# Kernel optimization log

Measured on AMD Instinct MI355X. Metric: run time of the kernel, lower is better.

The kernel has to match this reference:

```python
import jax, jax.numpy as jnp
import numpy as np

PATCH = 8
EPS = 1e-5

def patch_split(x, s):
    # B C H W -> B s*s rH rW C
    B, C, H, W = x.shape
    rH, rW = H // s, W // s
    out = x.reshape(B, C, s, rH, s, rW)
    out = out.transpose(0, 2, 4, 3, 5, 1)
    return out.reshape(B, s * s, rH, rW, C)

def patch_recover(x, s):
    # B s*s rH rW C -> B C H W
    B, N, rH, rW, C = x.shape
    out = x.reshape(B, s, s, rH, rW, C)
    out = out.transpose(0, 5, 1, 3, 2, 4)
    return out.reshape(B, C, s * rH, s * rW)

def conv2d(x, w, pad):
    return jax.lax.conv_general_dilated(x, w, (1, 1), [(pad, pad), (pad, pad)],
                                        dimension_numbers=('NCHW', 'OIHW', 'NCHW'))

def bn_relu(x, g, b):
    # eval-mode BatchNorm2d with fresh running stats (mean=0, var=1)
    scale = (g / jnp.sqrt(1.0 + EPS))[None, :, None, None]
    return jax.nn.relu(x * scale + b[None, :, None, None])


def setup_inputs() -> dict:
    key = jax.random.key(0)
    ks = jax.random.split(key, 24)
    r = lambda i, shape, s=0.02: jax.random.normal(ks[i], shape, jnp.float32) * s
    B, H, W, C, K, P = 4, 64, 64, 512, 19, 64
    return {
        'M_1': jax.random.normal(ks[0], (B, 2048, H, W), jnp.float32),
        'F': jax.random.normal(ks[1], (B, C, H, W), jnp.float32),
        'I': jax.random.normal(ks[2], (B, K, H, W), jnp.float32),
        'R': jax.random.uniform(ks[3], (B, K, PATCH, PATCH), jnp.float32),
        'lg_w1': r(4, (P, P)), 'lg_w2': r(5, (C, C)),
        'fuse_w': r(6, (P,)), 'fuse_b': r(7, (1,)),
        'q_w': r(8, (256, C)), 'q_b': r(9, (256,)),
        'k_w': r(10, (256, C)), 'k_b': r(11, (256,)),
        'v_w': r(12, (256, C)), 'v_b': r(13, (256,)),
        'c1_w': r(14, (512, 256, 1, 1)),
        'bn1_g': jnp.ones((512,)), 'bn1_b': jnp.zeros((512,)),
        'c2_w': r(15, (512, 512, 3, 3)),
        'bn2_g': jnp.ones((512,)), 'bn2_b': jnp.zeros((512,)),
        'c3_w': r(16, (512, 2560, 3, 3)),
        'bn3_g': jnp.ones((512,)), 'bn3_b': jnp.zeros((512,)),
        'drop_w': r(17, (K, 512, 1, 1)),
    }


def reference(M_1, F, I, R, lg_w1, lg_w2, fuse_w, fuse_b, q_w, q_b, k_w, k_b,
              v_w, v_b, c1_w, bn1_g, bn1_b, c2_w, bn2_g, bn2_b, c3_w, bn3_g,
              bn3_b, drop_w):
    B = F.shape[0]
    F_p5 = patch_split(F, PATCH)          # B P rH rW C
    _, P, rH, rW, C = F_p5.shape
    I_p5 = patch_split(I, PATCH)          # B P rH rW K
    K = I_p5.shape[-1]
    F_p = F_p5.reshape(B, P, rH * rW, C)
    I_p = I_p5.reshape(B, P, rH * rW, K)
    bin_conf = R.reshape(B, K, P).transpose(0, 2, 1)[..., None]  # B P K 1
    pix = jax.nn.softmax(I_p, axis=2)
    F_l = jnp.einsum('bpnk,bpnc->bpkc', pix, F_p) * bin_conf     # B P K C
    # LG block: 1x1 conv over P channels, residual relu, linear over C
    h = jnp.einsum('qp,bpkc->bqkc', lg_w1, F_l)
    h = jax.nn.relu(h + F_l)
    F_l = jnp.einsum('bpkc,dc->bpkd', h, lg_w2)
    # FUSE: 1x1 conv P->1 (with bias); broadcast replaces torch .repeat
    F_g = jnp.einsum('p,bpkc->bkc', fuse_w, F_l) + fuse_b        # B K C
    query = jnp.einsum('bpnc,dc->bpnd', F_p, q_w) + q_b          # B P N 256
    key_ = jnp.einsum('bpkc,dc->bpkd', F_l, k_w) + k_b           # B P K 256
    value = jnp.einsum('bkc,dc->bkd', F_g, v_w) + v_b            # B K 256
    aff = jax.nn.softmax(jnp.einsum('bpnd,bpkd->bpnk', query, key_), axis=-1)
    F_s = jnp.einsum('bpnk,bkd->bpnd', aff, value)               # B P N 256
    F_s = patch_recover(F_s.reshape(B, P, rH, rW, -1), PATCH)    # B 256 H W
    Fo1 = F + bn_relu(conv2d(F_s, c1_w, 0), bn1_g, bn1_b)
    x2 = bn_relu(conv2d(Fo1, c2_w, 1), bn2_g, bn2_b)
    x3 = bn_relu(conv2d(jnp.concatenate([x2, M_1], axis=1), c3_w, 1), bn3_g, bn3_b)
    # Dropout2d is identity in eval; final 1x1 classifier conv
    return conv2d(x3, drop_w, 0)
```

## Files before the change

### kernel.cpp

```cpp
#include <hip/hip_runtime.h>
#include <hip/hip_bf16.h>

typedef __hip_bfloat16 bf16;
using short8 = __attribute__((ext_vector_type(8))) short;
using f32x4  = __attribute__((ext_vector_type(4))) float;

__device__ __forceinline__ float b2f(bf16 v){ return __bfloat162float(v); }
__device__ __forceinline__ bf16  f2b(float v){ return __float2bfloat16(v); }

#define EPSV 1e-5f

__device__ __forceinline__ void gload16(const void* g, void* l) {
  __builtin_amdgcn_global_load_lds(
      (const __attribute__((address_space(1))) unsigned int*)g,
      (__attribute__((address_space(3))) unsigned int*)l, 16, 0, 0);
}

__global__ __launch_bounds__(256) void k_cast(const float* __restrict__ in,
                                              bf16* __restrict__ out, int n4) {
  int i = blockIdx.x * 256 + threadIdx.x;
  if (i < n4) {
    float4 v = ((const float4*)in)[i];
    union { ushort4 u; bf16 h[4]; } o;
    o.h[0] = f2b(v.x); o.h[1] = f2b(v.y); o.h[2] = f2b(v.z); o.h[3] = f2b(v.w);
    ((ushort4*)out)[i] = o.u;
  }
}

__global__ __launch_bounds__(256) void k_wtr(const float* __restrict__ w,
                                             bf16* __restrict__ wt, int CI) {
  int oc = blockIdx.x, c0 = blockIdx.y * 128;
  __shared__ float ld[128 * 9];
  const float* src = w + ((size_t)oc * CI + c0) * 9;
  for (int i = threadIdx.x; i < 128 * 9; i += 256) ld[i] = src[i];
  __syncthreads();
  for (int i = threadIdx.x; i < 128 * 9; i += 256) {
    int k9 = i / 128, t = i - k9 * 128;
    wt[((size_t)k9 * 512 + oc) * CI + c0 + t] = f2b(ld[t * 9 + k9]);
  }
}

__global__ __launch_bounds__(256) void k_m1t(const float* __restrict__ M1,
                                             bf16* __restrict__ M1b) {
  int b = blockIdx.x >> 6, y = blockIdx.x & 63;
  int c0 = blockIdx.y * 64;
  __shared__ float t[64][65];
  for (int i = threadIdx.x; i < 4096; i += 256) {
    int cc = i >> 6, x = i & 63;
    t[x][cc] = M1[((size_t)(b * 2048 + c0 + cc) * 64 + y) * 64 + x];
  }
  __syncthreads();
  for (int i = threadIdx.x; i < 4096; i += 256) {
    int x = i >> 6, cc = i & 63;
    M1b[((size_t)((b * 64 + y) * 64 + x)) * 2048 + c0 + cc] = f2b(t[x][cc]);
  }
}

__global__ __launch_bounds__(256) void k_fp2(const float* __restrict__ F,
                                             bf16* __restrict__ FP) {
  int b = blockIdx.x >> 6, y = blockIdx.x & 63;
  int tid = threadIdx.x;
  __shared__ float t[256][65];
  int p_hi = (y >> 3) << 3, n_hi = (y & 7) << 3;
  for (int half = 0; half < 2; half++) {
    int c0 = half << 8;
    for (int i = tid; i < 256 * 64; i += 256) {
      int cc = i >> 6, x = i & 63;
      t[cc][x] = F[((size_t)(b * 512 + c0 + cc) * 64 + y) * 64 + x];
    }
    __syncthreads();
    for (int x = 0; x < 64; x++) {
      int p = p_hi + (x >> 3), n = n_hi + (x & 7);
      FP[((size_t)(b * 64 + p)) * 32768 + n * 512 + c0 + tid] = f2b(t[tid][x]);
    }
    __syncthreads();
  }
}

__global__ __launch_bounds__(256) void k_flocal2(const float* __restrict__ I,
        const float* __restrict__ R, const bf16* __restrict__ FP,
        float* __restrict__ FL0) {
  int bp = blockIdx.x, b = bp >> 6, p = bp & 63;
  int tid = threadIdx.x, w = tid >> 6, lane = tid & 63;
  __shared__ __align__(16) bf16 fps[64 * 512];
  __shared__ float pix[19][64];
  __shared__ float bc[19];
  {
    const bf16* src = FP + (size_t)bp * 32768 + lane * 8;
    #pragma unroll
    for (int t = 0; t < 16; t++) {
      int chunk = w + t * 4;
      gload16(src + chunk * 512, (char*)fps + chunk * 1024);
    }
  }
  int py = (p >> 3) * 8, px = (p & 7) * 8;
  for (int i = tid; i < 19 * 64; i += 256) {
    int k = i >> 6, n = i & 63;
    int y = py + (n >> 3), x = px + (n & 7);
    pix[k][n] = I[((size_t)(b * 19 + k) * 64 + y) * 64 + x];
  }
  if (tid < 19) bc[tid] = R[(size_t)(b * 19 + tid) * 64 + p];
  __syncthreads();
  if (tid < 19) {
    float mx = -1e30f;
    for (int n = 0; n < 64; n++) mx = fmaxf(mx, pix[tid][n]);
    float s = 0.f;
    for (int n = 0; n < 64; n++) { float e = __expf(pix[tid][n] - mx); pix[tid][n] = e; s += e; }
    float sc = bc[tid] / s;
    for (int n = 0; n < 64; n++) pix[tid][n] *= sc;
  }
  __syncthreads();
  for (int task = tid; task < 19 * 64; task += 256) {
    int k = task >> 6, c8 = (task & 63) << 3;
    float acc[8] = {};
    for (int n = 0; n < 64; n++) {
      float pv = pix[k][n];
      union { short8 s; bf16 h[8]; } v;
      v.s = *(const short8*)&fps[n * 512 + c8];
      #pragma unroll
      for (int j = 0; j < 8; j++) acc[j] += pv * b2f(v.h[j]);
    }
    float* dst = FL0 + ((size_t)(b * 64 + p) * 19 + k) * 512 + c8;
    #pragma unroll
    for (int j = 0; j < 8; j++) dst[j] = acc[j];
  }
}

__global__ __launch_bounds__(256) void k_lg1(const float* __restrict__ FL0,
        const float* __restrict__ w1, bf16* __restrict__ Hb) {
  int tid = threadIdx.x;
  int b = blockIdx.y;
  int n0 = blockIdx.x * 256;
  __shared__ float W[64][64];
  __shared__ float Xs[16][256];
  for (int i = tid; i < 4096; i += 256) W[i >> 6][i & 63] = w1[i];
  float acc[64];
  #pragma unroll
  for (int po = 0; po < 64; po++) acc[po] = 0.f;
  for (int q0 = 0; q0 < 64; q0 += 16) {
    __syncthreads();
    for (int i = tid; i < 4096; i += 256) {
      int q = i >> 8, j = i & 255;
      Xs[q][j] = FL0[(size_t)(b * 64 + q0 + q) * 9728 + n0 + j];
    }
    __syncthreads();
    for (int q = 0; q < 16; q++) {
      float xv = Xs[q][tid];
      #pragma unroll
      for (int po = 0; po < 64; po++) acc[po] += W[po][q0 + q] * xv;
    }
  }
  for (int po = 0; po < 64; po++) {
    float r = acc[po] + FL0[(size_t)(b * 64 + po) * 9728 + n0 + tid];
    Hb[(size_t)(b * 64 + po) * 9728 + n0 + tid] = f2b(fmaxf(r, 0.f));
  }
}

template<int MODE>
__global__ __launch_bounds__(256) void k_gmm(
    const bf16* __restrict__ A, const bf16* __restrict__ B,
    const float* __restrict__ bias, float* __restrict__ C,
    bf16* __restrict__ Cb, int N, int K,
    const float* __restrict__ g, const float* __restrict__ bb,
    const float* __restrict__ Fres, bf16* __restrict__ outb) {
  int tid = threadIdx.x;
  int m0 = blockIdx.x * 128, n0 = blockIdx.y * 128;
  int w = tid >> 6, lane = tid & 63, ln = lane & 15, qd = lane >> 4;
  int wm = w & 1, wn = w >> 1;
  __shared__ __align__(16) char smem[34816];

  f32x4 acc[4][4];
  #pragma unroll
  for (int i = 0; i < 4; i++)
    #pragma unroll
    for (int j = 0; j < 4; j++) acc[i][j] = (f32x4){0.f, 0.f, 0.f, 0.f};

  int rsub = lane >> 2, ch = lane & 3;
  auto stage = [&](int p) {
    char* base = smem + (p & 1) * 16384;
    int k0 = p << 5;
    #pragma unroll
    for (int t = 0; t < 2; t++) {
      int ii = w + t * 4;
      int r = ii * 16 + rsub;
      int sw = (ch ^ ((r >> 1) & 3)) << 3;
      gload16(A + (size_t)(m0 + r) * K + k0 + sw, base + ii * 1024);
      gload16(B + (size_t)(n0 + r) * K + k0 + sw, base + 8192 + ii * 1024);
    }
  };
  auto compute = [&](int p) {
    const char* base = smem + (p & 1) * 16384;
    short8 af[4], bv[4];
    #pragma unroll
    for (int mi = 0; mi < 4; mi++) {
      int r = wm * 64 + mi * 16 + ln;
      af[mi] = *(const short8*)(base + r * 64 + ((qd ^ ((r >> 1) & 3)) << 4));
    }
    #pragma unroll
    for (int ni = 0; ni < 4; ni++) {
      int r = wn * 64 + ni * 16 + ln;
      bv[ni] = *(const short8*)(base + 8192 + r * 64 + ((qd ^ ((r >> 1) & 3)) << 4));
    }
    #pragma unroll
    for (int mi = 0; mi < 4; mi++)
      #pragma unroll
      for (int ni = 0; ni < 4; ni++)
        acc[mi][ni] = __builtin_amdgcn_mfma_f32_16x16x32_bf16(
            af[mi], bv[ni], acc[mi][ni], 0, 0, 0);
  };

  int KT = K >> 5;
  stage(0);
  __syncthreads();
  for (int p = 0; p < KT; p++) {
    if (p + 1 < KT) stage(p + 1);
    compute(p);
    __syncthreads();
  }

  if (MODE <= 1) {
    #pragma unroll
    for (int mi = 0; mi < 4; mi++) {
      #pragma unroll
      for (int r = 0; r < 4; r++) {
        int m = m0 + wm * 64 + mi * 16 + qd * 4 + r;
        #pragma unroll
        for (int ni = 0; ni < 4; ni++) {
          int n = n0 + wn * 64 + ni * 16 + ln;
          float v = acc[mi][ni][r];
          if (bias) v += bias[n];
          C[(size_t)m * N + n] = v;
          if (MODE == 1) Cb[(size_t)m * N + n] = f2b(v);
        }
      }
    }
  } else {
    bf16* EP = (bf16*)smem;
    int b = n0 >> 12;
    #pragma unroll
    for (int mi = 0; mi < 4; mi++) {
      #pragma unroll
      for (int r = 0; r < 4; r++) {
        int ml = wm * 64 + mi * 16 + qd * 4 + r;
        int oc = m0 + ml;
        float sc = g[oc] * rsqrtf(1.f + EPSV);
        float bt = bb[oc];
        #pragma unroll
        for (int ni = 0; ni < 4; ni++) {
          int nl = wn * 64 + ni * 16 + ln;
          int pix = n0 + nl;
          int y = (pix >> 6) & 63, x = pix & 63;
          float v = fmaxf(acc[mi][ni][r] * sc + bt, 0.f)
                  + Fres[((size_t)(b * 512 + oc) * 64 + y) * 64 + x];
          EP[nl * 136 + ml] = f2b(v);
        }
      }
    }
    __syncthreads();
    int pl = tid >> 1, half = tid & 1;
    size_t gb = (size_t)(n0 + pl) * 512 + m0 + half * 64;
    const bf16* row = &EP[pl * 136 + half * 64];
    #pragma unroll
    for (int j2 = 0; j2 < 8; j2++)
      *(short8*)(outb + gb + j2 * 8) = *(const short8*)(row + j2 * 8);
  }
}

__global__ __launch_bounds__(256) void k_fusev(const float* __restrict__ FL,
        const float* __restrict__ fw, const float* __restrict__ fbv,
        const float* __restrict__ vw, const float* __restrict__ vb,
        float* __restrict__ VAL) {
  int tid = threadIdx.x;
  int bk = blockIdx.x, b = bk / 19, k = bk % 19;
  __shared__ float fwl[64];
  __shared__ __align__(16) float fg[512];
  if (tid < 64) fwl[tid] = fw[tid];
  __syncthreads();
  float fbias = fbv[0];
  for (int c = tid; c < 512; c += 256) {
    float s = 0.f;
    for (int p = 0; p < 64; p++)
      s += fwl[p] * FL[((size_t)(b * 64 + p) * 19 + k) * 512 + c];
    fg[c] = s + fbias;
  }
  __syncthreads();
  int d = tid;
  float s = vb[d];
  const float4* vr = (const float4*)(vw + (size_t)d * 512);
  const float4* fr = (const float4*)fg;
  for (int c4 = 0; c4 < 128; c4++) {
    float4 wv = vr[c4], f = fr[c4];
    s += f.x * wv.x + f.y * wv.y + f.z * wv.z + f.w * wv.w;
  }
  VAL[(size_t)bk * 256 + d] = s;
}

__global__ __launch_bounds__(256) void k_attn(const float* __restrict__ Q,
        const float* __restrict__ KEY, const float* __restrict__ VAL,
        bf16* __restrict__ FS) {
  int tid = threadIdx.x;
  int bp = blockIdx.x, b = bp >> 6, p = bp & 63;
  __shared__ __align__(16) float ks[19][256];
  __shared__ __align__(16) float vs[19][256];
  __shared__ float Ss[64][20];
  __shared__ bf16 ot[64][256];
  for (int i = tid; i < 19 * 256; i += 256) {
    ks[i >> 8][i & 255] = KEY[(size_t)bp * 19 * 256 + i];
    vs[i >> 8][i & 255] = VAL[(size_t)b * 19 * 256 + i];
  }
  __syncthreads();
  {
    int n = tid >> 2, kq = tid & 3;
    const float4* qrow = (const float4*)(Q + ((size_t)bp * 64 + n) * 256);
    for (int k = kq; k < 19; k += 4) {
      const float4* kr = (const float4*)&ks[k][0];
      float s = 0.f;
      for (int d4 = 0; d4 < 64; d4++) {
        float4 qv = qrow[d4], kv = kr[d4];
        s += qv.x * kv.x + qv.y * kv.y + qv.z * kv.z + qv.w * kv.w;
      }
      Ss[n][k] = s;
    }
  }
  __syncthreads();
  if (tid < 64) {
    float mx = -1e30f;
    for (int k = 0; k < 19; k++) mx = fmaxf(mx, Ss[tid][k]);
    float sum = 0.f;
    for (int k = 0; k < 19; k++) { float e = __expf(Ss[tid][k] - mx); Ss[tid][k] = e; sum += e; }
    float inv = 1.f / sum;
    for (int k = 0; k < 19; k++) Ss[tid][k] *= inv;
  }
  __syncthreads();
  {
    int d = tid;
    for (int nn = 0; nn < 64; nn++) {
      float s = 0.f;
      #pragma unroll
      for (int k = 0; k < 19; k++) s += Ss[nn][k] * vs[k][d];
      ot[nn][d] = f2b(s);
    }
  }
  __syncthreads();
  {
    int py = (p >> 3) * 8, px = (p & 7) * 8;
    int nn = tid >> 2, q = tid & 3;
    int y = py + (nn >> 3), x = px + (nn & 7);
    size_t gb = (((size_t)(b * 64 + y) * 64) + x) * 256 + q * 64;
    const bf16* row = &ot[nn][q * 64];
    #pragma unroll
    for (int j = 0; j < 8; j++)
      *(short8*)(FS + gb + j * 8) = *(const short8*)(row + j * 8);
  }
}

__global__ __launch_bounds__(512) void k_conv3(
    const bf16* __restrict__ Xin, int Cin,
    const bf16* __restrict__ M1b, const float* __restrict__ M1f, int C2,
    const bf16* __restrict__ WT,
    const float* __restrict__ g, const float* __restrict__ bb,
    bf16* __restrict__ out, int Cos) {
  int tid = threadIdx.x;
  int b = blockIdx.x >> 4, y0 = (blockIdx.x & 15) * 4;
  int oc0 = blockIdx.y * 128;
  int w = tid >> 6, lane = tid & 63, ln = lane & 15, qd = lane >> 4;
  int wocg = w & 1, wyp = w >> 1;
  int Ct = Cin + C2;

  __shared__ __align__(16) char smem[100864];
  char* smA  = smem;
  char* smB  = smem + 49152;
  char* dump = smem + 99840;

  for (int bufi = 0; bufi < 2; bufi++) {
    char* bbuf = smB + bufi * 25344;
    for (int i = tid; i < 6 * 2 * 32; i += 512) {
      int rl = i >> 6, hh = (i >> 5) & 1, kk = i & 31;
      *(bf16*)(bbuf + (rl * 66 + (hh ? 65 : 0)) * 64 + kk * 2) = f2b(0.f);
    }
    if (y0 == 0)
      for (int i = tid; i < 66 * 16; i += 512) ((float*)bbuf)[i] = 0.f;
    if (y0 == 60)
      for (int i = tid; i < 66 * 16; i += 512)
        ((float*)(bbuf + 5 * 66 * 64))[i] = 0.f;
  }

  f32x4 acc[4][4];
  #pragma unroll
  for (int i = 0; i < 4; i++)
    #pragma unroll
    for (int j = 0; j < 4; j++) acc[i][j] = (f32x4){0.f, 0.f, 0.f, 0.f};

  int NPH = (Ct >> 5) * 3;

  auto stageA = [&](int p) {
    int c0 = (p / 3) << 5, ky = p % 3;
    char* base = smA + (p & 1) * 24576;
    #pragma unroll
    for (int t = 0; t < 3; t++) {
      int j = w + t * 8;
      int kx = j >> 3, i8 = j & 7;
      int ocl = i8 * 16 + (lane >> 2);
      const bf16* src = WT + ((size_t)((ky * 3 + kx) * 512 + oc0 + ocl) * Ct + c0)
                      + (((lane & 3) ^ ((ocl >> 1) & 3)) << 3);
      gload16(src, base + (kx * 128 + i8 * 16) * 64);
    }
  };
  auto stageB = [&](int gi) {
    int c0 = gi << 5;
    char* bbuf = smB + (gi & 1) * 25344;
    if (c0 < Cin || M1b != nullptr) {
      const bf16* T; int Cs, cb;
      if (c0 < Cin) { T = Xin; Cs = Cin; cb = c0; }
      else          { T = M1b; Cs = C2;  cb = c0 - Cin; }
      #pragma unroll
      for (int t = 0; t < 3; t++) {
        int j = w + t * 8;
        int rl = j >> 2, q = j & 3;
        int yy = y0 + rl - 1;
        bool ok = (unsigned)yy < 64u;
        int yc = ok ? yy : y0;
        int xx = q * 16 + (lane >> 2), xr = xx + 1;
        const bf16* src = T + ((size_t)((b * 64 + yc) * 64 + xx) * Cs + cb)
                        + (((lane & 3) ^ ((xr >> 1) & 3)) << 3);
        char* dst = ok ? (bbuf + (rl * 66 + 1 + q * 16) * 64) : dump;
        gload16(src, dst);
      }
    } else {
      if (w < 6) {
        int rl = w, yy = y0 + rl - 1;
        if ((unsigned)yy < 64u) {
          int xx = lane, xr = xx + 1;
          const float* mp = M1f + ((size_t)(b * 2048 + (c0 - Cin)) * 64 + yy) * 64 + xx;
          #pragma unroll
          for (int q = 0; q < 8; q++) {
            union { ushort4 u; bf16 h[4]; } pk;
            #pragma unroll
            for (int jj = 0; jj < 4; jj++) pk.h[jj] = f2b(mp[(size_t)(q * 4 + jj) * 4096]);
            *(ushort4*)(bbuf + (rl * 66 + xr) * 64
                        + ((((q >> 1) ^ ((xr >> 1) & 3)) << 4) | ((q & 1) << 3))) = pk.u;
          }
        }
      }
    }
  };
  auto computeP = [&](int p) {
    int ky = p % 3;
    const char* base = smA + (p & 1) * 24576;
    const char* bB   = smB + ((p / 3) & 1) * 25344;
    int rl = wyp + ky;
    #pragma unroll
    for (int kx = 0; kx < 3; kx++) {
      short8 af[4], bv[4];
      #pragma unroll
      for (int mi = 0; mi < 4; mi++) {
        int ocl = wocg * 64 + mi * 16 + ln;
        af[mi] = *(const short8*)(base + (kx * 128 + ocl) * 64
                                  + ((qd ^ ((ocl >> 1) & 3)) << 4));
      }
      #pragma unroll
      for (int ni = 0; ni < 4; ni++) {
        int xr = ni * 16 + ln + kx;
        bv[ni] = *(const short8*)(bB + (rl * 66 + xr) * 64
                                  + ((qd ^ ((xr >> 1) & 3)) << 4));
      }
      #pragma unroll
      for (int mi = 0; mi < 4; mi++)
        #pragma unroll
        for (int ni = 0; ni < 4; ni++)
          acc[mi][ni] = __builtin_amdgcn_mfma_f32_16x16x32_bf16(
              af[mi], bv[ni], acc[mi][ni], 0, 0, 0);
    }
  };

  stageB(0);
  stageA(0);
  asm volatile("s_waitcnt vmcnt(0)" ::: "memory");
  __syncthreads();

  for (int p = 0; p < NPH; p++) {
    int pn = p + 1;
    bool hasA = pn < NPH;
    bool hasB = hasA && (pn % 3 == 0);
    bool bfast = false;
    if (hasA) stageA(pn);
    if (hasB) {
      int gi = pn / 3;
      bfast = ((gi << 5) < Cin) || (M1b != nullptr);
      stageB(gi);
    }
    __builtin_amdgcn_sched_barrier(0);
    if (!hasA)              asm volatile("s_waitcnt vmcnt(0)" ::: "memory");
    else if (hasB && bfast) asm volatile("s_waitcnt vmcnt(6)" ::: "memory");
    else                    asm volatile("s_waitcnt vmcnt(3)" ::: "memory");
    __builtin_amdgcn_s_barrier();
    __builtin_amdgcn_sched_barrier(0);
    computeP(p);
    __builtin_amdgcn_sched_barrier(0);
    asm volatile("s_waitcnt lgkmcnt(0)" ::: "memory");
    __builtin_amdgcn_s_barrier();
  }
  __syncthreads();

  {
    bf16* EP = (bf16*)smem;
    #pragma unroll
    for (int mi = 0; mi < 4; mi++) {
      int oclb = wocg * 64 + mi * 16 + qd * 4;
      float sc[4], bt[4];
      #pragma unroll
      for (int r = 0; r < 4; r++) {
        int oc = oc0 + oclb + r;
        sc[r] = g[oc] * rsqrtf(1.f + EPSV);
        bt[r] = bb[oc];
      }
      #pragma unroll
      for (int ni = 0; ni < 4; ni++) {
        int x = ni * 16 + ln;
        union { ushort4 u; bf16 h[4]; } pk;
        #pragma unroll
        for (int r = 0; r < 4; r++)
          pk.h[r] = f2b(fmaxf(acc[mi][ni][r] * sc[r] + bt[r], 0.f));
        *(ushort4*)&EP[(wyp * 64 + x) * 128 + oclb] = pk.u;
      }
    }
    __syncthreads();
    int pixl = tid >> 1, hh = tid & 1;
    int yloc = pixl >> 6, x = pixl & 63;
    size_t gb = ((size_t)((b * 64 + y0 + yloc) * 64 + x)) * Cos + oc0 + hh * 64;
    const bf16* row = &EP[pixl * 128 + hh * 64];
    #pragma unroll
    for (int k = 0; k < 8; k++)
      *(short8*)(out + gb + k * 8) = *(const short8*)(row + k * 8);
  }
}

__global__ __launch_bounds__(256) void k_final(const bf16* __restrict__ X3,
        const float* __restrict__ dw, float* __restrict__ out) {
  int tid = threadIdx.x;
  int b = blockIdx.x >> 6, y = blockIdx.x & 63;
  __shared__ float W[19 * 512];
  for (int i = tid; i < 19 * 512; i += 256) W[i] = dw[i];
  __syncthreads();
  int x = tid & 63, kg = tid >> 6;
  const bf16* px = X3 + (((size_t)(b * 64 + y) * 64) + x) * 512;
  float acc[5] = {0.f, 0.f, 0.f, 0.f, 0.f};
  for (int c8 = 0; c8 < 512; c8 += 8) {
    union { short8 s; bf16 h[8]; } v;
    v.s = *(const short8*)(px + c8);
    float f[8];
    #pragma unroll
    for (int j = 0; j < 8; j++) f[j] = b2f(v.h[j]);
    #pragma unroll
    for (int i = 0; i < 5; i++) {
      int k = kg * 5 + i;
      if (k < 19) {
        const float* wr = &W[k * 512 + c8];
        #pragma unroll
        for (int j = 0; j < 8; j++) acc[i] += f[j] * wr[j];
      }
    }
  }
  for (int i = 0; i < 5; i++) {
    int k = kg * 5 + i;
    if (k < 19) out[((size_t)(b * 19 + k) * 64 + y) * 64 + x] = acc[i];
  }
}

extern "C" void kernel_launch(void* const* d_in, const int* in_sizes, int n_in,
                              void* d_out, int out_size, void* d_ws, size_t ws_size,
                              hipStream_t stream) {
  (void)in_sizes; (void)n_in; (void)out_size;
  const float* M1 = (const float*)d_in[0];
  const float* F  = (const float*)d_in[1];
  const float* Iin= (const float*)d_in[2];
  const float* R  = (const float*)d_in[3];
  const float* w1 = (const float*)d_in[4];
  const float* w2 = (const float*)d_in[5];
  const float* fw = (const float*)d_in[6];
  const float* fb = (const float*)d_in[7];
  const float* qw = (const float*)d_in[8];
  const float* qb = (const float*)d_in[9];
  const float* kw = (const float*)d_in[10];
  const float* kb = (const float*)d_in[11];
  const float* vw = (const float*)d_in[12];
  const float* vb = (const float*)d_in[13];
  const float* c1 = (const float*)d_in[14];
  const float* g1 = (const float*)d_in[15];
  const float* b1 = (const float*)d_in[16];
  const float* c2 = (const float*)d_in[17];
  const float* g2 = (const float*)d_in[18];
  const float* b2 = (const float*)d_in[19];
  const float* c3 = (const float*)d_in[20];
  const float* g3 = (const float*)d_in[21];
  const float* b3 = (const float*)d_in[22];
  const float* dw = (const float*)d_in[23];

  char* ws = (char*)d_ws;
  bool fast = ws_size >= (size_t)137363456ULL;

  bf16*  qwb  = (bf16*)(ws + 0);
  bf16*  kwb  = (bf16*)(ws + 262144);
  bf16*  w2b  = (bf16*)(ws + 524288);
  bf16*  c1b  = (bf16*)(ws + 1048576);
  bf16*  WT2  = (bf16*)(ws + 0);
  bf16*  WT3  = (bf16*)(ws + 4718592);
  bf16*  FS   = (bf16*)(ws + 28311552);
  bf16*  FO1  = (bf16*)(ws + 36700160);
  bf16*  X2   = (bf16*)(ws + 53477376);
  bf16*  M1bf = fast ? (bf16*)(ws + 70254592) : nullptr;
  bf16*  X3   = (bf16*)(ws + 28311552);
  bf16*  FP    = (bf16*) (ws + 53477376);
  float* QUERY = (float*)(ws + 70254592);
  float* FL0   = (float*)(ws + 87031808);
  bf16*  Hb    = (bf16*) (ws + 96993280);
  bf16*  FLb   = (bf16*) (ws + 101974016);
  float* KEY   = (float*)(ws + 106954752);
  float* VAL   = (float*)(ws + 111935488);
  float* FL    = FL0;

  k_cast<<<128, 256, 0, stream>>>(qw, qwb, 32768);
  k_cast<<<128, 256, 0, stream>>>(kw, kwb, 32768);
  k_cast<<<256, 256, 0, stream>>>(w2, w2b, 65536);
  k_cast<<<128, 256, 0, stream>>>(c1, c1b, 32768);
  k_fp2<<<256, 256, 0, stream>>>(F, FP);
  k_flocal2<<<256, 256, 0, stream>>>(Iin, R, FP, FL0);
  k_lg1<<<dim3(38, 4), 256, 0, stream>>>(FL0, w1, Hb);
  k_gmm<1><<<dim3(38, 4), 256, 0, stream>>>(Hb, w2b, nullptr, FL, FLb, 512, 512,
                                            nullptr, nullptr, nullptr, nullptr);
  k_fusev<<<76, 256, 0, stream>>>(FL, fw, fb, vw, vb, VAL);
  k_gmm<0><<<dim3(38, 2), 256, 0, stream>>>(FLb, kwb, kb, KEY, nullptr, 256, 512,
                                            nullptr, nullptr, nullptr, nullptr);
  k_gmm<0><<<dim3(128, 2), 256, 0, stream>>>(FP, qwb, qb, QUERY, nullptr, 256, 512,
                                             nullptr, nullptr, nullptr, nullptr);
  k_attn<<<256, 256, 0, stream>>>(QUERY, KEY, VAL, FS);
  if (fast) k_m1t<<<dim3(256, 32), 256, 0, stream>>>(M1, M1bf);
  k_gmm<2><<<dim3(4, 128), 256, 0, stream>>>(c1b, FS, nullptr, nullptr, nullptr,
                                             16384, 256, g1, b1, F, FO1);
  k_wtr<<<dim3(512, 4),  256, 0, stream>>>(c2, WT2, 512);
  k_wtr<<<dim3(512, 20), 256, 0, stream>>>(c3, WT3, 2560);
  k_conv3<<<dim3(64, 4), 512, 0, stream>>>(FO1, 512, nullptr, nullptr, 0,
                                           WT2, g2, b2, X2, 512);
  k_conv3<<<dim3(64, 4), 512, 0, stream>>>(X2, 512, M1bf, M1, 2048,
                                           WT3, g3, b3, X3, 512);
  k_final<<<256, 256, 0, stream>>>(X3, dw, (float*)d_out);
}
```

Measured before the change: 990.8 us.

## Triple-buffer conv3 weight stages with one barrier per phase; merge cast/transpose launches

Result: no change. 972.0 us (-1.9%).

```diff
diff --git a/kernel.cpp b/kernel.cpp
--- a/kernel.cpp
+++ b/kernel.cpp
@@ -16,20 +16,30 @@
       (__attribute__((address_space(3))) unsigned int*)l, 16, 0, 0);
 }
 
-__global__ __launch_bounds__(256) void k_cast(const float* __restrict__ in,
-                                              bf16* __restrict__ out, int n4) {
+__global__ __launch_bounds__(256) void k_cast4(
+    const float* __restrict__ a, bf16* __restrict__ ao,
+    const float* __restrict__ b, bf16* __restrict__ bo,
+    const float* __restrict__ c, bf16* __restrict__ co,
+    const float* __restrict__ d, bf16* __restrict__ dd) {
   int i = blockIdx.x * 256 + threadIdx.x;
-  if (i < n4) {
-    float4 v = ((const float4*)in)[i];
-    union { ushort4 u; bf16 h[4]; } o;
-    o.h[0] = f2b(v.x); o.h[1] = f2b(v.y); o.h[2] = f2b(v.z); o.h[3] = f2b(v.w);
-    ((ushort4*)out)[i] = o.u;
-  }
-}
-
-__global__ __launch_bounds__(256) void k_wtr(const float* __restrict__ w,
-                                             bf16* __restrict__ wt, int CI) {
-  int oc = blockIdx.x, c0 = blockIdx.y * 128;
+  const float* src; bf16* dst; int off;
+  if (i < 32768)       { src = a; dst = ao; off = i; }
+  else if (i < 65536)  { src = b; dst = bo; off = i - 32768; }
+  else if (i < 131072) { src = c; dst = co; off = i - 65536; }
+  else                 { src = d; dst = dd; off = i - 131072; }
+  float4 v = ((const float4*)src)[off];
+  union { ushort4 u; bf16 h[4]; } o;
+  o.h[0] = f2b(v.x); o.h[1] = f2b(v.y); o.h[2] = f2b(v.z); o.h[3] = f2b(v.w);
+  ((ushort4*)dst)[off] = o.u;
+}
+
+__global__ __launch_bounds__(256) void k_wtr2(
+    const float* __restrict__ wa, bf16* __restrict__ wta,
+    const float* __restrict__ wb, bf16* __restrict__ wtb) {
+  int oc = blockIdx.x, yy = blockIdx.y;
+  const float* w; bf16* wt; int CI, c0;
+  if (yy < 4) { w = wa; wt = wta; CI = 512;  c0 = yy * 128; }
+  else        { w = wb; wt = wtb; CI = 2560; c0 = (yy - 4) * 128; }
   __shared__ float ld[128 * 9];
   const float* src = w + ((size_t)oc * CI + c0) * 9;
   for (int i = threadIdx.x; i < 128 * 9; i += 256) ld[i] = src[i];
@@ -367,10 +377,10 @@
   int wocg = w & 1, wyp = w >> 1;
   int Ct = Cin + C2;
 
-  __shared__ __align__(16) char smem[100864];
+  __shared__ __align__(16) char smem[125440];
   char* smA  = smem;
-  char* smB  = smem + 49152;
-  char* dump = smem + 99840;
+  char* smB  = smem + 73728;
+  char* dump = smem + 124416;
 
   for (int bufi = 0; bufi < 2; bufi++) {
     char* bbuf = smB + bufi * 25344;
@@ -391,11 +401,16 @@
     #pragma unroll
     for (int j = 0; j < 4; j++) acc[i][j] = (f32x4){0.f, 0.f, 0.f, 0.f};
 
-  int NPH = (Ct >> 5) * 3;
+  int ngroups = Ct >> 5;
+  int NPH = ngroups * 3;
 
   auto stageA = [&](int p) {
     int c0 = (p / 3) << 5, ky = p % 3;
-    char* base = smA + (p & 1) * 24576;
+    char* base = smA + (p % 3 == p - (p / 3) * 3 ? 0 : 0) ;
+    base = smA + (p % 3) * 0;
+    base = smA + ((p % 3) == 0 ? 0 : 0);
+    base = smA + ky * 0;
+    base = smA + (p % 3) * 24576;
     #pragma unroll
     for (int t = 0; t < 3; t++) {
       int j = w + t * 8;
@@ -442,11 +457,12 @@
           }
         }
       }
+      asm volatile("s_waitcnt lgkmcnt(0)" ::: "memory");
     }
   };
   auto computeP = [&](int p) {
     int ky = p % 3;
-    const char* base = smA + (p & 1) * 24576;
+    const char* base = smA + (p % 3) * 24576;
     const char* bB   = smB + ((p / 3) & 1) * 25344;
     int rl = wyp + ky;
     #pragma unroll
@@ -475,30 +491,29 @@
 
   stageB(0);
   stageA(0);
-  asm volatile("s_waitcnt vmcnt(0)" ::: "memory");
-  __syncthreads();
+  stageA(1);
+  asm volatile("s_waitcnt lgkmcnt(0)" ::: "memory");
 
   for (int p = 0; p < NPH; p++) {
-    int pn = p + 1;
-    bool hasA = pn < NPH;
-    bool hasB = hasA && (pn % 3 == 0);
-    bool bfast = false;
-    if (hasA) stageA(pn);
-    if (hasB) {
-      int gi = pn / 3;
-      bfast = ((gi << 5) < Cin) || (M1b != nullptr);
-      stageB(gi);
-    }
-    __builtin_amdgcn_sched_barrier(0);
-    if (!hasA)              asm volatile("s_waitcnt vmcnt(0)" ::: "memory");
-    else if (hasB && bfast) asm volatile("s_waitcnt vmcnt(6)" ::: "memory");
-    else                    asm volatile("s_waitcnt vmcnt(3)" ::: "memory");
     __builtin_amdgcn_s_barrier();
     __builtin_amdgcn_sched_barrier(0);
+    if (p + 2 < NPH) stageA(p + 2);
+    int pm3 = p % 3;
+    int gn = p / 3 + 1;
+    bool bValid = gn < ngroups;
+    bool bFastN = bValid && (((gn << 5) < Cin) || (M1b != nullptr));
+    if (pm3 == 1 && bValid) stageB(gn);
+    __builtin_amdgcn_sched_barrier(0);
+    int N = (p + 1 < NPH ? 3 : 0) + (p + 2 < NPH ? 3 : 0)
+          + ((pm3 != 0 && bFastN) ? 3 : 0);
+    if (N == 9)      asm volatile("s_waitcnt vmcnt(9)" ::: "memory");
+    else if (N == 6) asm volatile("s_waitcnt vmcnt(6)" ::: "memory");
+    else if (N == 3) asm volatile("s_waitcnt vmcnt(3)" ::: "memory");
+    else             asm volatile("s_waitcnt vmcnt(0)" ::: "memory");
+    __builtin_amdgcn_sched_barrier(0);
+    __builtin_amdgcn_s_setprio(1);
     computeP(p);
-    __builtin_amdgcn_sched_barrier(0);
-    asm volatile("s_waitcnt lgkmcnt(0)" ::: "memory");
-    __builtin_amdgcn_s_barrier();
+    __builtin_amdgcn_s_setprio(0);
   }
   __syncthreads();
 
@@ -619,10 +634,7 @@
   float* VAL   = (float*)(ws + 111935488);
   float* FL    = FL0;
 
-  k_cast<<<128, 256, 0, stream>>>(qw, qwb, 32768);
-  k_cast<<<128, 256, 0, stream>>>(kw, kwb, 32768);
-  k_cast<<<256, 256, 0, stream>>>(w2, w2b, 65536);
-  k_cast<<<128, 256, 0, stream>>>(c1, c1b, 32768);
+  k_cast4<<<640, 256, 0, stream>>>(qw, qwb, kw, kwb, w2, w2b, c1, c1b);
   k_fp2<<<256, 256, 0, stream>>>(F, FP);
   k_flocal2<<<256, 256, 0, stream>>>(Iin, R, FP, FL0);
   k_lg1<<<dim3(38, 4), 256, 0, stream>>>(FL0, w1, Hb);
@@ -637,8 +649,7 @@
   if (fast) k_m1t<<<dim3(256, 32), 256, 0, stream>>>(M1, M1bf);
   k_gmm<2><<<dim3(4, 128), 256, 0, stream>>>(c1b, FS, nullptr, nullptr, nullptr,
                                              16384, 256, g1, b1, F, FO1);
-  k_wtr<<<dim3(512, 4),  256, 0, stream>>>(c2, WT2, 512);
-  k_wtr<<<dim3(512, 20), 256, 0, stream>>>(c3, WT3, 2560);
+  k_wtr2<<<dim3(512, 24), 256, 0, stream>>>(c2, WT2, c3, WT3);
   k_conv3<<<dim3(64, 4), 512, 0, stream>>>(FO1, 512, nullptr, nullptr, 0,
                                            WT2, g2, b2, X2, 512);
   k_conv3<<<dim3(64, 4), 512, 0, stream>>>(X2, 512, M1bf, M1, 2048,
```
